# Kernel optimization log

Measured on AMD Instinct MI355X. Metric: run time of the kernel, lower is better.

Reference implementation:

```python
import jax, jax.numpy as jnp
import numpy as np
import math

V, H, NH, L, S, B = 100000, 2048, 64, 2, 512, 2
HD = H // NH  # 32
MAX_LEN = 5000
EPS_NORM = 1e-5
EPS_ATTN = 1e-6


def build_pe():
    # PositionalEncoding buffer: pe[max_len, 1, d_model]
    position = jnp.arange(MAX_LEN, dtype=jnp.float32)[:, None]
    div_term = jnp.exp(jnp.arange(0, H, 2, dtype=jnp.float32) * (-math.log(10000.0) / H))
    ang = position * div_term  # [max_len, H/2]
    pe = jnp.zeros((MAX_LEN, 1, H), dtype=jnp.float32)
    pe = pe.at[:, 0, 0::2].set(jnp.sin(ang))
    pe = pe.at[:, 0, 1::2].set(jnp.cos(ang))
    return pe


def fast_inv_sqrt(x):
    # Quake fast inverse sqrt; the bit-trick seed is detached in the original
    x2 = x * 0.5
    i = jax.lax.bitcast_convert_type(jax.lax.stop_gradient(x.astype(jnp.float32)), jnp.int32)
    i = jnp.int32(1597463007) - (i >> 1)
    y = jax.lax.bitcast_convert_type(i, jnp.float32)
    return y * (1.5 - x2 * y * y)  # grad flows only through x2, as in torch


def sr_norm(h, w, b):
    mean = h.mean(-1, keepdims=True)
    var = ((h - mean) ** 2).mean(-1, keepdims=True)  # biased variance
    inv = fast_inv_sqrt(var + EPS_NORM)
    return w * ((h - mean) * inv) + b


def attn_layer(x, wq, bq, wk, bk, wv, bv, wo, bo, nw, nb):
    # x: [B, S, H]; weights stored [in, out]
    def heads(t):
        return t.reshape(B, S, NH, HD).transpose(0, 2, 1, 3)  # [B, NH, S, HD]
    q = heads(x @ wq + bq)
    k = heads(x @ wk + bk)
    v = heads(x @ wv + bv)
    scores = jnp.einsum('bhqd,bhkd->bhqk', q, k) / math.sqrt(HD)
    a = jax.nn.softmax(scores, axis=-1)
    # dropout is identity in eval; then double softmax (exp/sum) + sigmoid gate
    e = jnp.exp(a)
    a2 = e / (e.sum(-1, keepdims=True) + EPS_ATTN)
    cw = a2 * jax.nn.sigmoid(a2)
    o = jnp.einsum('bhqk,bhkd->bhqd', cw, v)
    o = o.transpose(0, 2, 1, 3).reshape(B, S, H)
    o = o @ wo + bo
    return sr_norm(o + x, nw, nb)


def setup_inputs():
    key = jax.random.key(0)
    ks = jax.random.split(key, 12)
    def rn(k, shape):
        return jax.random.normal(k, shape, dtype=jnp.float32) * 0.02
    return {
        'src': jax.random.randint(ks[0], (B, S), 0, V),
        'emb': jax.random.uniform(ks[1], (V, H), minval=-0.1, maxval=0.1, dtype=jnp.float32),
        'Wq': rn(ks[2], (L, H, H)), 'bq': jnp.zeros((L, H), jnp.float32),
        'Wk': rn(ks[3], (L, H, H)), 'bk': jnp.zeros((L, H), jnp.float32),
        'Wv': rn(ks[4], (L, H, H)), 'bv': jnp.zeros((L, H), jnp.float32),
        'Wo': rn(ks[5], (L, H, H)), 'bo': jnp.zeros((L, H), jnp.float32),
        'nw': jnp.ones((L, H), jnp.float32), 'nb': jnp.zeros((L, H), jnp.float32),
        'Wout': jax.random.uniform(ks[6], (H, V), minval=-0.1, maxval=0.1, dtype=jnp.float32),
        'bout': jnp.zeros((V,), jnp.float32),
    }


def reference(src, emb, Wq, bq, Wk, bk, Wv, bv, Wo, bo, nw, nb, Wout, bout):
    x = emb[src] * math.sqrt(H)  # [B, S, H]
    pe = build_pe()
    # Faithful to pe[:x.size(0)] where x is [B, S, H]: indexes by BATCH dim
    x = x + pe[:x.shape[0]]  # [B, 1, H] broadcast over seq
    for l in range(L):
        x = attn_layer(x, Wq[l], bq[l], Wk[l], bk[l], Wv[l], bv[l],
                       Wo[l], bo[l], nw[l], nb[l])
    return x @ Wout + bout  # [B, S, V]
```

## Files before the change

### kernel.cpp

```cpp
#include <hip/hip_runtime.h>


#define DEVINL __device__ __forceinline__

typedef float f32x4 __attribute__((ext_vector_type(4)));
typedef __bf16 bf16x8 __attribute__((ext_vector_type(8)));
typedef __bf16 bf16x2v __attribute__((ext_vector_type(2)));

DEVINL unsigned int pk2(float a, float b) {
  bf16x2v v;
  v[0] = (__bf16)a;
  v[1] = (__bf16)b;
  return __builtin_bit_cast(unsigned int, v);
}

DEVINL unsigned short bf1(float a) {
  __bf16 v = (__bf16)a;
  return __builtin_bit_cast(unsigned short, v);
}

DEVINL void gload_lds16(const void* g, void* l) {
  __builtin_amdgcn_global_load_lds(
      (const __attribute__((address_space(1))) unsigned int*)g,
      (__attribute__((address_space(3))) unsigned int*)l, 16, 0, 0);
}

__global__ __launch_bounds__(256) void embed_kernel(
    const int* __restrict__ src, const float* __restrict__ emb,
    float* __restrict__ x, unsigned short* __restrict__ xbf) {
  const int row = blockIdx.x;
  const int b = row >> 9;
  const int tok = src[row];
  const float sqrtH = 45.25483399593904f;
  const float c = -9.210340371976184f / 2048.f;
  for (int h = threadIdx.x; h < 2048; h += 256) {
    int i = h >> 1;
    float dv = expf((float)(2 * i) * c);
    float ang = (float)b * dv;
    float pe = (h & 1) ? cosf(ang) : sinf(ang);
    float val = emb[(size_t)tok * 2048 + h] * sqrtH + pe;
    x[(size_t)row * 2048 + h] = val;
    xbf[(size_t)row * 2048 + h] = bf1(val);
  }
}

__global__ __launch_bounds__(256) void wtrans_kernel(
    const float* __restrict__ W, unsigned short* __restrict__ WT, const int N) {
  __shared__ float t[64][65];
  const int tid = threadIdx.x;
  const int n0 = blockIdx.x * 64, k0 = blockIdx.y * 64;
  const int c4 = (tid & 15) * 4;
#pragma unroll
  for (int it = 0; it < 4; ++it) {
    int kl = it * 16 + (tid >> 4);
    int n = n0 + c4;
    float4 wv;
    if (n + 3 < N) {
      wv = *(const float4*)(W + (size_t)(k0 + kl) * N + n);
    } else {
      wv.x = (n + 0 < N) ? W[(size_t)(k0 + kl) * N + n + 0] : 0.f;
      wv.y = (n + 1 < N) ? W[(size_t)(k0 + kl) * N + n + 1] : 0.f;
      wv.z = (n + 2 < N) ? W[(size_t)(k0 + kl) * N + n + 2] : 0.f;
      wv.w = (n + 3 < N) ? W[(size_t)(k0 + kl) * N + n + 3] : 0.f;
    }
    t[kl][c4 + 0] = wv.x;
    t[kl][c4 + 1] = wv.y;
    t[kl][c4 + 2] = wv.z;
    t[kl][c4 + 3] = wv.w;
  }
  __syncthreads();
  const int kp = (tid & 15) * 4;
#pragma unroll
  for (int j = 0; j < 4; ++j) {
    int nl = j * 16 + (tid >> 4);
    uint2 u = make_uint2(pk2(t[kp + 0][nl], t[kp + 1][nl]),
                         pk2(t[kp + 2][nl], t[kp + 3][nl]));
    *(uint2*)&WT[(size_t)(n0 + nl) * 2048 + k0 + kp] = u;
  }
}

template <int BM, int NN>
DEVINL void gemm_bf_body(const unsigned short* __restrict__ A,
                         const unsigned short* __restrict__ BT,
                         const float* __restrict__ bias, float* __restrict__ C,
                         const int m0, const int n0) {
  constexpr int K = 2048;
  constexpr int WM = BM / 32;
  __shared__ __align__(16) unsigned short A_lds[2][BM * 32];
  __shared__ __align__(16) unsigned short B_lds[2][128 * 32];

  const int tid = threadIdx.x;
  const int w = tid >> 6, lane = tid & 63;
  const int wm = w >> 1, wn = w & 1;

  const int aRow = lane >> 2;
  const int aChunk = (lane & 3) ^ ((lane >> 3) & 3);

  int aOff[WM], bOff[4];
#pragma unroll
  for (int mi = 0; mi < WM; ++mi) {
    int m = wm * (BM / 2) + mi * 16 + (lane & 15);
    aOff[mi] = m * 32 + ((lane >> 4) ^ ((m >> 1) & 3)) * 8;
  }
#pragma unroll
  for (int ni = 0; ni < 4; ++ni) {
    int n = wn * 64 + ni * 16 + (lane & 15);
    bOff[ni] = n * 32 + ((lane >> 4) ^ ((n >> 1) & 3)) * 8;
  }

  f32x4 acc[WM][4] = {};

  auto stage = [&](int k0, int bf) {
#pragma unroll
    for (int i = 0; i < BM / 64; ++i) {
      int r0 = (w * (BM / 64) + i) * 16;
      gload_lds16(A + (size_t)(m0 + r0 + aRow) * K + k0 + aChunk * 8, &A_lds[bf][r0 * 32]);
    }
#pragma unroll
    for (int i = 0; i < 2; ++i) {
      int r0 = (w * 2 + i) * 16;
      gload_lds16(BT + (size_t)(n0 + r0 + aRow) * K + k0 + aChunk * 8, &B_lds[bf][r0 * 32]);
    }
  };
  auto compute = [&](int bf) {
    bf16x8 af[WM], bfr[4];
#pragma unroll
    for (int mi = 0; mi < WM; ++mi) af[mi] = *(const bf16x8*)&A_lds[bf][aOff[mi]];
#pragma unroll
    for (int ni = 0; ni < 4; ++ni) bfr[ni] = *(const bf16x8*)&B_lds[bf][bOff[ni]];
#pragma unroll
    for (int mi = 0; mi < WM; ++mi)
#pragma unroll
      for (int ni = 0; ni < 4; ++ni)
        acc[mi][ni] = __builtin_amdgcn_mfma_f32_16x16x32_bf16(af[mi], bfr[ni], acc[mi][ni], 0, 0, 0);
  };

  stage(0, 0);
  __syncthreads();
  int buf = 0;
  for (int t = 0; t < K / 32 - 1; ++t) {
    stage((t + 1) * 32, buf ^ 1);
    compute(buf);
    __syncthreads();
    buf ^= 1;
  }
  compute(buf);

  const int r0w = (lane >> 4) * 4;
  const int lrow = lane & 15;
#pragma unroll
  for (int mi = 0; mi < WM; ++mi)
#pragma unroll
    for (int ni = 0; ni < 4; ++ni) {
      int ccol = n0 + wn * 64 + ni * 16 + lrow;
      if ((NN % 128 == 0) || ccol < NN) {
        float bv = bias[ccol];
#pragma unroll
        for (int r = 0; r < 4; ++r) {
          int crow = m0 + wm * (BM / 2) + mi * 16 + r0w + r;
          C[(size_t)crow * NN + ccol] = acc[mi][ni][r] + bv;
        }
      }
    }
}

template <int BM, int NN>
__global__ __launch_bounds__(256) void gemm_bf_kernel(
    const unsigned short* __restrict__ A, const unsigned short* __restrict__ BT,
    const float* __restrict__ bias, float* __restrict__ C) {
  gemm_bf_body<BM, NN>(A, BT, bias, C, blockIdx.x * BM, blockIdx.y * 128);
}

__global__ __launch_bounds__(256) void gemm_qkv_bf_kernel(
    const unsigned short* __restrict__ A, const unsigned short* __restrict__ WT,
    const float* __restrict__ bq, const float* __restrict__ bk, const float* __restrict__ bv,
    float* __restrict__ q, float* __restrict__ k, float* __restrict__ v) {
  const int z = blockIdx.z;
  const unsigned short* BT = WT + (size_t)z * 2048 * 2048;
  const float* bias = (z == 0) ? bq : (z == 1) ? bk : bv;
  float* C = (z == 0) ? q : (z == 1) ? k : v;
  gemm_bf_body<64, 2048>(A, BT, bias, C, blockIdx.x * 64, blockIdx.y * 128);
}

__global__ __launch_bounds__(256) void gemm_final_bf_kernel(
    const unsigned short* __restrict__ A, const unsigned short* __restrict__ BT,
    const float* __restrict__ bias, float* __restrict__ C) {
  const int bid = blockIdx.x;
  const int f = (bid & 7) * (gridDim.x >> 3) + (bid >> 3);
  gemm_bf_body<128, 100000>(A, BT, bias, C, (f & 7) * 128, (f >> 3) * 128);
}

template <int BM>
DEVINL void gemm_body(const unsigned short* __restrict__ A, const float* __restrict__ B,
                      const float* __restrict__ bias, float* __restrict__ C,
                      const int N, const int m0, const int n0) {
  constexpr int K = 2048;
  constexpr int WM = BM / 32;
  constexpr int AI = BM / 64;
  __shared__ __align__(16) unsigned short A_lds[2][BM * 32];
  __shared__ __align__(16) unsigned short B_lds[2][128 * 32];

  const int tid = threadIdx.x;
  const int w = tid >> 6, lane = tid & 63;
  const int wm = w >> 1, wn = w & 1;

  const int n_local = tid & 127;
  const int kq = tid >> 7;
  const int col = n0 + n_local;
  const bool colok = col < N;
  const int bswz = (n_local >> 1) & 3;

  const int aRow = lane >> 2;
  const int aChunk = (lane & 3) ^ ((lane >> 3) & 3);

  int aOff[WM], bOff[4];
#pragma unroll
  for (int mi = 0; mi < WM; ++mi) {
    int m = wm * (BM / 2) + mi * 16 + (lane & 15);
    aOff[mi] = m * 32 + ((lane >> 4) ^ ((m >> 1) & 3)) * 8;
  }
#pragma unroll
  for (int ni = 0; ni < 4; ++ni) {
    int n = wn * 64 + ni * 16 + (lane & 15);
    bOff[ni] = n * 32 + ((lane >> 4) ^ ((n >> 1) & 3)) * 8;
  }

  f32x4 acc[WM][4] = {};
  float fB[16];

  auto stageA = [&](int k0, int bf) {
#pragma unroll
    for (int i = 0; i < AI; ++i) {
      int r0 = (w * AI + i) * 16;
      gload_lds16(A + (size_t)(m0 + r0 + aRow) * K + k0 + aChunk * 8, &A_lds[bf][r0 * 32]);
    }
  };
  auto loadB = [&](int k0) {
#pragma unroll
    for (int g = 0; g < 4; ++g) {
      int kl = (g * 2 + kq) * 4;
#pragma unroll
      for (int i = 0; i < 4; ++i)
        fB[g * 4 + i] = colok ? B[(size_t)(k0 + kl + i) * N + col] : 0.f;
    }
  };
  auto writeB = [&](int bf) {
#pragma unroll
    for (int g = 0; g < 4; ++g) {
      int kl = (g * 2 + kq) * 4;
      uint2 p = make_uint2(pk2(fB[g * 4 + 0], fB[g * 4 + 1]),
                           pk2(fB[g * 4 + 2], fB[g * 4 + 3]));
      int chunk = (kl >> 3) ^ bswz;
      *(uint2*)&B_lds[bf][n_local * 32 + chunk * 8 + (kl & 7)] = p;
    }
  };
  auto compute = [&](int bf) {
    bf16x8 af[WM], bfr[4];
#pragma unroll
    for (int mi = 0; mi < WM; ++mi) af[mi] = *(const bf16x8*)&A_lds[bf][aOff[mi]];
#pragma unroll
    for (int ni = 0; ni < 4; ++ni) bfr[ni] = *(const bf16x8*)&B_lds[bf][bOff[ni]];
#pragma unroll
    for (int mi = 0; mi < WM; ++mi)
#pragma unroll
      for (int ni = 0; ni < 4; ++ni)
        acc[mi][ni] = __builtin_amdgcn_mfma_f32_16x16x32_bf16(af[mi], bfr[ni], acc[mi][ni], 0, 0, 0);
  };

  stageA(0, 0);
  loadB(0);
  writeB(0);
  __syncthreads();
  int buf = 0;
  for (int t = 0; t < K / 32 - 1; ++t) {
    stageA((t + 1) * 32, buf ^ 1);
    loadB((t + 1) * 32);
    compute(buf);
    writeB(buf ^ 1);
    __syncthreads();
    buf ^= 1;
  }
  compute(buf);

  const int r0w = (lane >> 4) * 4;
  const int lrow = lane & 15;
#pragma unroll
  for (int mi = 0; mi < WM; ++mi)
#pragma unroll
    for (int ni = 0; ni < 4; ++ni) {
      int ccol = n0 + wn * 64 + ni * 16 + lrow;
      if (ccol < N) {
        float bv = bias[ccol];
#pragma unroll
        for (int r = 0; r < 4; ++r) {
          int crow = m0 + wm * (BM / 2) + mi * 16 + r0w + r;
          C[(size_t)crow * N + ccol] = acc[mi][ni][r] + bv;
        }
      }
    }
}

__global__ __launch_bounds__(256) void gemm_qkv_kernel(
    const unsigned short* __restrict__ A,
    const float* __restrict__ Wq, const float* __restrict__ Wk, const float* __restrict__ Wv,
    const float* __restrict__ bq, const float* __restrict__ bk, const float* __restrict__ bv,
    float* __restrict__ q, float* __restrict__ k, float* __restrict__ v) {
  const int z = blockIdx.z;
  const float* B = (z == 0) ? Wq : (z == 1) ? Wk : Wv;
  const float* bias = (z == 0) ? bq : (z == 1) ? bk : bv;
  float* C = (z == 0) ? q : (z == 1) ? k : v;
  gemm_body<64>(A, B, bias, C, 2048, blockIdx.x * 64, blockIdx.y * 128);
}

template <int BM>
__global__ __launch_bounds__(256) void gemm_kernel(
    const unsigned short* __restrict__ A, const float* __restrict__ B,
    const float* __restrict__ bias, float* __restrict__ C, const int N) {
  gemm_body<BM>(A, B, bias, C, N, blockIdx.x * BM, blockIdx.y * 128);
}

__global__ __launch_bounds__(256) void gemm_final_kernel(
    const unsigned short* __restrict__ A, const float* __restrict__ B,
    const float* __restrict__ bias, float* __restrict__ C, const int N) {
  const int bid = blockIdx.x;
  const int f = (bid & 7) * (gridDim.x >> 3) + (bid >> 3);
  gemm_body<128>(A, B, bias, C, N, (f & 7) * 128, (f >> 3) * 128);
}

__global__ __launch_bounds__(256) void attn_kernel(
    const float* __restrict__ q, const float* __restrict__ k,
    const float* __restrict__ v, unsigned short* __restrict__ o) {
  __shared__ __align__(16) float K_lds[512 * 32];
  const int tid = threadIdx.x;
  const int blk = blockIdx.x;
  const int bh = blk >> 2, chunk = blk & 3;
  const int b = bh >> 6, h = bh & 63;
  const size_t headoff = (size_t)b * 512 * 2048 + (size_t)h * 32;

  const float* kb = k + headoff;
#pragma unroll
  for (int i = 0; i < 16; ++i) {
    int flat = i * 256 + tid;
    int j = flat >> 3, d4 = flat & 7;
    *(float4*)&K_lds[j * 32 + d4 * 4] = *(const float4*)(kb + (size_t)j * 2048 + d4 * 4);
  }
  __syncthreads();

  const int row = chunk * 128 + (tid >> 1);
  const int half = tid & 1;
  const int j0 = half * 256, j1 = j0 + 256;
  const float* qr = q + headoff + (size_t)row * 2048;
  float4 Q[8];
#pragma unroll
  for (int d = 0; d < 8; ++d) Q[d] = *(const float4*)(qr + d * 4);

  const float scale = 0.17677669529663689f;
  auto dot = [&](int j) -> float {
    const float4* kr = (const float4*)&K_lds[j * 32];
    float p0 = 0.f, p1 = 0.f, p2 = 0.f, p3 = 0.f;
#pragma unroll
    for (int d = 0; d < 8; ++d) {
      float4 kk = kr[d];
      p0 = fmaf(Q[d].x, kk.x, p0);
      p1 = fmaf(Q[d].y, kk.y, p1);
      p2 = fmaf(Q[d].z, kk.z, p2);
      p3 = fmaf(Q[d].w, kk.w, p3);
    }
    return ((p0 + p1) + (p2 + p3)) * scale;
  };

  float m = -1e30f, denom = 0.f;
  for (int j = j0; j < j1; ++j) {
    float s = dot(j);
    float nm = fmaxf(m, s);
    denom = denom * __expf(m - nm) + __expf(s - nm);
    m = nm;
  }
  {
    float m2 = __shfl_xor(m, 1);
    float d2 = __shfl_xor(denom, 1);
    float mm = fmaxf(m, m2);
    denom = denom * __expf(m - mm) + d2 * __expf(m2 - mm);
    m = mm;
  }
  const float invd = 1.f / denom;

  float sum_e = 0.f;
  for (int j = j0; j < j1; ++j) {
    float a = __expf(dot(j) - m) * invd;
    sum_e += __expf(a);
  }
  sum_e += __shfl_xor(sum_e, 1);
  const float inv_se = 1.f / (sum_e + 1e-6f);

  float4 accv[8];
#pragma unroll
  for (int d = 0; d < 8; ++d) accv[d] = make_float4(0.f, 0.f, 0.f, 0.f);
  const float* vb = v + headoff;
  float4 vcur[8];
#pragma unroll
  for (int d = 0; d < 8; ++d) vcur[d] = *(const float4*)(vb + (size_t)j0 * 2048 + d * 4);
  for (int j = j0; j < j1; ++j) {
    float4 vnxt[8];
    if (j + 1 < j1) {
      const float4* vr = (const float4*)(vb + (size_t)(j + 1) * 2048);
#pragma unroll
      for (int d = 0; d < 8; ++d) vnxt[d] = vr[d];
    } else {
#pragma unroll
      for (int d = 0; d < 8; ++d) vnxt[d] = vcur[d];
    }
    float a = __expf(dot(j) - m) * invd;
    float e = __expf(a);
    float a2 = e * inv_se;
    float cw = a2 / (1.f + __expf(-a2));
#pragma unroll
    for (int d = 0; d < 8; ++d) {
      accv[d].x = fmaf(cw, vcur[d].x, accv[d].x);
      accv[d].y = fmaf(cw, vcur[d].y, accv[d].y);
      accv[d].z = fmaf(cw, vcur[d].z, accv[d].z);
      accv[d].w = fmaf(cw, vcur[d].w, accv[d].w);
    }
#pragma unroll
    for (int d = 0; d < 8; ++d) vcur[d] = vnxt[d];
  }
#pragma unroll
  for (int d = 0; d < 8; ++d) {
    accv[d].x += __shfl_xor(accv[d].x, 1);
    accv[d].y += __shfl_xor(accv[d].y, 1);
    accv[d].z += __shfl_xor(accv[d].z, 1);
    accv[d].w += __shfl_xor(accv[d].w, 1);
  }
  unsigned short* orow = o + headoff + (size_t)row * 2048;
#pragma unroll
  for (int g = 0; g < 4; ++g) {
    int d = half * 4 + g;
    uint2 p = make_uint2(pk2(accv[d].x, accv[d].y), pk2(accv[d].z, accv[d].w));
    *(uint2*)&orow[d * 4] = p;
  }
}

__global__ __launch_bounds__(256) void norm_kernel(
    const float* __restrict__ o, const float* __restrict__ xin,
    const float* __restrict__ w, const float* __restrict__ bb,
    float* __restrict__ xout, unsigned short* __restrict__ xbf) {
  __shared__ float red[4];
  const int row = blockIdx.x, tid = threadIdx.x;
  const float* op = o + (size_t)row * 2048;
  const float* xp = xin + (size_t)row * 2048;
  float4 hv[2];
#pragma unroll
  for (int i = 0; i < 2; ++i) {
    float4 a = *(const float4*)(op + tid * 4 + i * 1024);
    float4 c = *(const float4*)(xp + tid * 4 + i * 1024);
    hv[i] = make_float4(a.x + c.x, a.y + c.y, a.z + c.z, a.w + c.w);
  }
  float s = 0.f;
#pragma unroll
  for (int i = 0; i < 2; ++i) s += hv[i].x + hv[i].y + hv[i].z + hv[i].w;
  for (int off = 32; off; off >>= 1) s += __shfl_down(s, off);
  if ((tid & 63) == 0) red[tid >> 6] = s;
  __syncthreads();
  const float mean = (red[0] + red[1] + red[2] + red[3]) * (1.f / 2048.f);
  __syncthreads();

  float vs = 0.f;
#pragma unroll
  for (int i = 0; i < 2; ++i) {
    float dx = hv[i].x - mean, dy = hv[i].y - mean, dz = hv[i].z - mean, dw = hv[i].w - mean;
    vs += dx * dx + dy * dy + dz * dz + dw * dw;
  }
  for (int off = 32; off; off >>= 1) vs += __shfl_down(vs, off);
  if ((tid & 63) == 0) red[tid >> 6] = vs;
  __syncthreads();
  const float var = (red[0] + red[1] + red[2] + red[3]) * (1.f / 2048.f);

  const float xv = var + 1e-5f;
  int ii = __float_as_int(xv);
  ii = 1597463007 - (ii >> 1);
  float y = __int_as_float(ii);
  y = y * (1.5f - 0.5f * xv * y * y);

#pragma unroll
  for (int i = 0; i < 2; ++i) {
    int c0 = tid * 4 + i * 1024;
    float4 wv = *(const float4*)(w + c0);
    float4 bv = *(const float4*)(bb + c0);
    float r0 = wv.x * ((hv[i].x - mean) * y) + bv.x;
    float r1 = wv.y * ((hv[i].y - mean) * y) + bv.y;
    float r2 = wv.z * ((hv[i].z - mean) * y) + bv.z;
    float r3 = wv.w * ((hv[i].w - mean) * y) + bv.w;
    *(float4*)(xout + (size_t)row * 2048 + c0) = make_float4(r0, r1, r2, r3);
    *(uint2*)&xbf[(size_t)row * 2048 + c0] = make_uint2(pk2(r0, r1), pk2(r2, r3));
  }
}

extern "C" void kernel_launch(void* const* d_in, const int* in_sizes, int n_in,
                              void* d_out, int out_size, void* d_ws, size_t ws_size,
                              hipStream_t stream) {
  const int*   src  = (const int*)d_in[0];
  const float* emb  = (const float*)d_in[1];
  const float* Wq   = (const float*)d_in[2];
  const float* bq   = (const float*)d_in[3];
  const float* Wk   = (const float*)d_in[4];
  const float* bk   = (const float*)d_in[5];
  const float* Wv   = (const float*)d_in[6];
  const float* bv   = (const float*)d_in[7];
  const float* Wo   = (const float*)d_in[8];
  const float* bo   = (const float*)d_in[9];
  const float* nw   = (const float*)d_in[10];
  const float* nb   = (const float*)d_in[11];
  const float* Wout = (const float*)d_in[12];
  const float* bout = (const float*)d_in[13];
  float* out = (float*)d_out;

  char* ws = (char*)d_ws;
  float* x  = (float*)(ws);
  float* qb = (float*)(ws + (8ll << 20));
  float* kb = (float*)(ws + (16ll << 20));
  float* vb = (float*)(ws + (24ll << 20));
  float* ob = (float*)(ws + (32ll << 20));
  unsigned short* xbf = (unsigned short*)(ws + (40ll << 20));
  unsigned short* abf = (unsigned short*)(ws + (44ll << 20));

  const unsigned long long NEED = (112ull << 20) + 100096ull * 2048ull * 2ull;
  const bool big = (unsigned long long)ws_size >= NEED;
  unsigned short* WTp = (unsigned short*)(ws + (48ll << 20));
  unsigned short* WTo = (unsigned short*)(ws + (112ll << 20));

  embed_kernel<<<1024, 256, 0, stream>>>(src, emb, x, xbf);

  if (big) {
    for (int l = 0; l < 2; ++l) {
      const size_t wo_ = (size_t)l * 2048 * 2048;
      const float* Wm[4] = {Wq + wo_, Wk + wo_, Wv + wo_, Wo + wo_};
      for (int mt = 0; mt < 4; ++mt)
        wtrans_kernel<<<dim3(32, 32), 256, 0, stream>>>(
            Wm[mt], WTp + (size_t)(l * 4 + mt) * 2048 * 2048, 2048);
    }
    wtrans_kernel<<<dim3(1564, 32), 256, 0, stream>>>(Wout, WTo, 100000);

    for (int l = 0; l < 2; ++l) {
      const size_t bo_ = (size_t)l * 2048;
      const unsigned short* WTl = WTp + (size_t)(l * 4) * 2048 * 2048;
      gemm_qkv_bf_kernel<<<dim3(16, 16, 3), 256, 0, stream>>>(
          xbf, WTl, bq + bo_, bk + bo_, bv + bo_, qb, kb, vb);
      attn_kernel<<<512, 256, 0, stream>>>(qb, kb, vb, abf);
      gemm_bf_kernel<64, 2048><<<dim3(16, 16), 256, 0, stream>>>(
          abf, WTl + (size_t)3 * 2048 * 2048, bo + bo_, ob);
      norm_kernel<<<1024, 256, 0, stream>>>(ob, x, nw + bo_, nb + bo_, x, xbf);
    }
    gemm_final_bf_kernel<<<8 * 782, 256, 0, stream>>>(xbf, WTo, bout, out);
  } else {
    for (int l = 0; l < 2; ++l) {
      const size_t wo_ = (size_t)l * 2048 * 2048;
      const size_t bo_ = (size_t)l * 2048;
      gemm_qkv_kernel<<<dim3(16, 16, 3), 256, 0, stream>>>(
          xbf, Wq + wo_, Wk + wo_, Wv + wo_, bq + bo_, bk + bo_, bv + bo_, qb, kb, vb);
      attn_kernel<<<512, 256, 0, stream>>>(qb, kb, vb, abf);
      gemm_kernel<64><<<dim3(16, 16), 256, 0, stream>>>(abf, Wo + wo_, bo + bo_, ob, 2048);
      norm_kernel<<<1024, 256, 0, stream>>>(ob, x, nw + bo_, nb + bo_, x, xbf);
    }
    gemm_final_kernel<<<8 * 782, 256, 0, stream>>>(xbf, Wout, bout, out, 100000);
  }
}
```

Before: 1.839 ms.

## Triple-buffer GEMM pipeline, enlarge QKV tile, precompute PE, widen transpose stores

The bf16 GEMM body moves from double to triple buffering, using explicit vmcnt waits and a single barrier per k-step so global-to-LDS loads run two stages ahead of compute. The QKV GEMM uses 128-row tiles, which halves its grid. The positional encoding is computed once into a small table, and the embed kernel now does vectorized float4 loads and stores. The weight-transpose kernel writes 16-byte packed stores instead of 8-byte ones. These changes raise LDS use per block, which may reduce occupancy, and the final 100000-column GEMM, which dominates runtime, only benefits through the shared pipeline change.

```diff
diff --git a/kernel.cpp b/kernel.cpp
--- a/kernel.cpp
+++ b/kernel.cpp
@@ -14,33 +14,40 @@
   return __builtin_bit_cast(unsigned int, v);
 }
 
-DEVINL unsigned short bf1(float a) {
-  __bf16 v = (__bf16)a;
-  return __builtin_bit_cast(unsigned short, v);
-}
-
 DEVINL void gload_lds16(const void* g, void* l) {
   __builtin_amdgcn_global_load_lds(
       (const __attribute__((address_space(1))) unsigned int*)g,
       (__attribute__((address_space(3))) unsigned int*)l, 16, 0, 0);
 }
 
+__global__ __launch_bounds__(256) void peinit_kernel(float* __restrict__ pe_tab) {
+  const int h = blockIdx.x * 256 + threadIdx.x;
+  const float c = -9.210340371976184f / 2048.f;
+  const int i = h >> 1;
+  const float dv = expf((float)(2 * i) * c);
+#pragma unroll
+  for (int b = 0; b < 2; ++b) {
+    float ang = (float)b * dv;
+    pe_tab[b * 2048 + h] = (h & 1) ? cosf(ang) : sinf(ang);
+  }
+}
+
 __global__ __launch_bounds__(256) void embed_kernel(
     const int* __restrict__ src, const float* __restrict__ emb,
-    float* __restrict__ x, unsigned short* __restrict__ xbf) {
+    const float* __restrict__ pe_tab, float* __restrict__ x, unsigned short* __restrict__ xbf) {
   const int row = blockIdx.x;
   const int b = row >> 9;
   const int tok = src[row];
   const float sqrtH = 45.25483399593904f;
-  const float c = -9.210340371976184f / 2048.f;
-  for (int h = threadIdx.x; h < 2048; h += 256) {
-    int i = h >> 1;
-    float dv = expf((float)(2 * i) * c);
-    float ang = (float)b * dv;
-    float pe = (h & 1) ? cosf(ang) : sinf(ang);
-    float val = emb[(size_t)tok * 2048 + h] * sqrtH + pe;
-    x[(size_t)row * 2048 + h] = val;
-    xbf[(size_t)row * 2048 + h] = bf1(val);
+  const float* er = emb + (size_t)tok * 2048;
+  const float* pr = pe_tab + b * 2048;
+  for (int c0 = threadIdx.x * 4; c0 < 2048; c0 += 1024) {
+    float4 e = *(const float4*)(er + c0);
+    float4 p = *(const float4*)(pr + c0);
+    float r0 = fmaf(e.x, sqrtH, p.x), r1 = fmaf(e.y, sqrtH, p.y);
+    float r2 = fmaf(e.z, sqrtH, p.z), r3 = fmaf(e.w, sqrtH, p.w);
+    *(float4*)(x + (size_t)row * 2048 + c0) = make_float4(r0, r1, r2, r3);
+    *(uint2*)&xbf[(size_t)row * 2048 + c0] = make_uint2(pk2(r0, r1), pk2(r2, r3));
   }
 }
 
@@ -69,13 +76,16 @@
     t[kl][c4 + 3] = wv.w;
   }
   __syncthreads();
-  const int kp = (tid & 15) * 4;
-#pragma unroll
-  for (int j = 0; j < 4; ++j) {
-    int nl = j * 16 + (tid >> 4);
-    uint2 u = make_uint2(pk2(t[kp + 0][nl], t[kp + 1][nl]),
-                         pk2(t[kp + 2][nl], t[kp + 3][nl]));
-    *(uint2*)&WT[(size_t)(n0 + nl) * 2048 + k0 + kp] = u;
+  const int kp = (tid & 7) * 8;
+#pragma unroll
+  for (int j = 0; j < 2; ++j) {
+    int nl = j * 32 + (tid >> 3);
+    uint4 u;
+    u.x = pk2(t[kp + 0][nl], t[kp + 1][nl]);
+    u.y = pk2(t[kp + 2][nl], t[kp + 3][nl]);
+    u.z = pk2(t[kp + 4][nl], t[kp + 5][nl]);
+    u.w = pk2(t[kp + 6][nl], t[kp + 7][nl]);
+    *(uint4*)&WT[(size_t)(n0 + nl) * 2048 + k0 + kp] = u;
   }
 }
 
@@ -85,9 +95,11 @@
                          const float* __restrict__ bias, float* __restrict__ C,
                          const int m0, const int n0) {
   constexpr int K = 2048;
+  constexpr int NT = K / 32;
   constexpr int WM = BM / 32;
-  __shared__ __align__(16) unsigned short A_lds[2][BM * 32];
-  __shared__ __align__(16) unsigned short B_lds[2][128 * 32];
+  constexpr int LP = BM / 64 + 2;
+  __shared__ __align__(16) unsigned short A_lds[3][BM * 32];
+  __shared__ __align__(16) unsigned short B_lds[3][128 * 32];
 
   const int tid = threadIdx.x;
   const int w = tid >> 6, lane = tid & 63;
@@ -136,15 +148,16 @@
   };
 
   stage(0, 0);
-  __syncthreads();
-  int buf = 0;
-  for (int t = 0; t < K / 32 - 1; ++t) {
-    stage((t + 1) * 32, buf ^ 1);
-    compute(buf);
-    __syncthreads();
-    buf ^= 1;
-  }
-  compute(buf);
+  stage(32, 1);
+  for (int t = 0; t < NT - 1; ++t) {
+    asm volatile("s_waitcnt vmcnt(%0)" :: "i"(LP) : "memory");
+    __builtin_amdgcn_s_barrier();
+    if (t < NT - 2) stage((t + 2) * 32, (t + 2) % 3);
+    compute(t % 3);
+  }
+  asm volatile("s_waitcnt vmcnt(0)" ::: "memory");
+  __builtin_amdgcn_s_barrier();
+  compute((NT - 1) % 3);
 
   const int r0w = (lane >> 4) * 4;
   const int lrow = lane & 15;
@@ -179,7 +192,7 @@
   const unsigned short* BT = WT + (size_t)z * 2048 * 2048;
   const float* bias = (z == 0) ? bq : (z == 1) ? bk : bv;
   float* C = (z == 0) ? q : (z == 1) ? k : v;
-  gemm_bf_body<64, 2048>(A, BT, bias, C, blockIdx.x * 64, blockIdx.y * 128);
+  gemm_bf_body<128, 2048>(A, BT, bias, C, blockIdx.x * 128, blockIdx.y * 128);
 }
 
 __global__ __launch_bounds__(256) void gemm_final_bf_kernel(
@@ -522,13 +535,15 @@
   float* ob = (float*)(ws + (32ll << 20));
   unsigned short* xbf = (unsigned short*)(ws + (40ll << 20));
   unsigned short* abf = (unsigned short*)(ws + (44ll << 20));
+  float* pe_tab = ob;
 
   const unsigned long long NEED = (112ull << 20) + 100096ull * 2048ull * 2ull;
   const bool big = (unsigned long long)ws_size >= NEED;
   unsigned short* WTp = (unsigned short*)(ws + (48ll << 20));
   unsigned short* WTo = (unsigned short*)(ws + (112ll << 20));
 
-  embed_kernel<<<1024, 256, 0, stream>>>(src, emb, x, xbf);
+  peinit_kernel<<<8, 256, 0, stream>>>(pe_tab);
+  embed_kernel<<<1024, 256, 0, stream>>>(src, emb, pe_tab, x, xbf);
 
   if (big) {
     for (int l = 0; l < 2; ++l) {
@@ -543,7 +558,7 @@
     for (int l = 0; l < 2; ++l) {
       const size_t bo_ = (size_t)l * 2048;
       const unsigned short* WTl = WTp + (size_t)(l * 4) * 2048 * 2048;
-      gemm_qkv_bf_kernel<<<dim3(16, 16, 3), 256, 0, stream>>>(
+      gemm_qkv_bf_kernel<<<dim3(8, 16, 3), 256, 0, stream>>>(
           xbf, WTl, bq + bo_, bk + bo_, bv + bo_, qb, kb, vb);
       attn_kernel<<<512, 256, 0, stream>>>(qb, kb, vb, abf);
       gemm_bf_kernel<64, 2048><<<dim3(16, 16), 256, 0, stream>>>(
```

Result: slower. 1.957 ms (+6.4%).
